# Kernel optimization log

Measured on AMD Instinct MI355X. Metric: run time of the kernel, lower is better.

## Reference

```python
import jax, jax.numpy as jnp
import numpy as np

KERNEL_SIZE = 3

def setup_inputs() -> dict:
    key = jax.random.key(0)
    x = jax.random.normal(key, (16, 64, 128, 128), dtype=jnp.float32)
    return {"x": x}

def reference(x) -> jnp.ndarray:
    # im2col / sliding-window patch extraction with zero padding (SAME).
    # out[b, h, w, c, i, j] = pad(x)[b, c, h + i, w + j]
    k = KERNEL_SIZE
    p = k // 2
    B, C, H, W = x.shape
    xp = jnp.pad(x, ((0, 0), (0, 0), (p, p), (p, p)))  # (B, C, H+2p, W+2p)
    # k*k = 9 static slices (not a data-dim loop), stacked into one tensor.
    patches = jnp.stack(
        [xp[:, :, i:i + H, j:j + W] for i in range(k) for j in range(k)],
        axis=-1,
    )  # (B, C, H, W, k*k)
    patches = patches.reshape(B, C, H, W, k, k)
    return patches.transpose(0, 2, 3, 1, 4, 5)  # (B, H, W, C, k, k)
```

## Files before the change

### kernel.cpp

```cpp
#include <hip/hip_runtime.h>


typedef float f4 __attribute__((ext_vector_type(4), aligned(4)));

__global__ __launch_bounds__(576)
void im2col_kernel(const float* __restrict__ x, float* __restrict__ out) {
    const int el = threadIdx.x;

    const int bid = blockIdx.x;
    const int R   = ((bid & 7) << 8) + (bid >> 3);
    const int h = R & 127;
    const int b = R >> 7;

    const int c  = el / 9;
    const int ij = el - c * 9;
    const int i  = ij / 3;
    const int j  = ij - i * 3;

    const int row = h + i - 1;
    const bool rv = (unsigned)row < 128u;
    const float* rp = x + ((size_t)b * 64 + c) * 16384 + (rv ? row : 0) * 128;
    const int j1 = j - 1;

    float* ob = out + (size_t)R * (128 * 576) + el;

    {
        int col = j1;
        float v = rp[col < 0 ? 0 : col];
        __builtin_nontemporal_store((rv && col >= 0) ? v : 0.0f, ob);
    }

#pragma unroll 4
    for (int it = 0; it < 31; ++it) {
        int w = 1 + (it << 2);
        f4 v = *(const f4*)(rp + w + j1);
        if (!rv) { v.x = 0.0f; v.y = 0.0f; v.z = 0.0f; v.w = 0.0f; }
        float* o = ob + (size_t)w * 576;
        __builtin_nontemporal_store(v.x, o);
        __builtin_nontemporal_store(v.y, o + 576);
        __builtin_nontemporal_store(v.z, o + 2 * 576);
        __builtin_nontemporal_store(v.w, o + 3 * 576);
    }

#pragma unroll
    for (int w = 125; w < 128; ++w) {
        int col = w + j1;
        float v = rp[col > 127 ? 127 : col];
        __builtin_nontemporal_store((rv && col <= 127) ? v : 0.0f,
                                    ob + (size_t)w * 576);
    }
}

extern "C" void kernel_launch(void* const* d_in, const int* in_sizes, int n_in,
                              void* d_out, int out_size, void* d_ws, size_t ws_size,
                              hipStream_t stream) {
    const float* x = (const float*)d_in[0];
    float* out = (float*)d_out;
    im2col_kernel<<<2048, 576, 0, stream>>>(x, out);
}
```

Baseline: 120.2 us.

## Vectorize output stores by assigning four consecutive channel-patch elements per thread

```diff
diff --git a/kernel.cpp b/kernel.cpp
--- a/kernel.cpp
+++ b/kernel.cpp
@@ -5,49 +5,66 @@
 
 __global__ __launch_bounds__(576)
 void im2col_kernel(const float* __restrict__ x, float* __restrict__ out) {
-    const int el = threadIdx.x;
-
+    const int tid = threadIdx.x;
     const int bid = blockIdx.x;
     const int R   = ((bid & 7) << 8) + (bid >> 3);
     const int h = R & 127;
     const int b = R >> 7;
 
-    const int c  = el / 9;
-    const int ij = el - c * 9;
-    const int i  = ij / 3;
-    const int j  = ij - i * 3;
+    const int p0 = tid / 144;
+    const int q  = tid - p0 * 144;
 
-    const int row = h + i - 1;
-    const bool rv = (unsigned)row < 128u;
-    const float* rp = x + ((size_t)b * 64 + c) * 16384 + (rv ? row : 0) * 128;
-    const int j1 = j - 1;
-
-    float* ob = out + (size_t)R * (128 * 576) + el;
-
-    {
-        int col = j1;
-        float v = rp[col < 0 ? 0 : col];
-        __builtin_nontemporal_store((rv && col >= 0) ? v : 0.0f, ob);
+    const float* ptr[4];
+    int jm1[4];
+    bool rv[4];
+#pragma unroll
+    for (int u = 0; u < 4; ++u) {
+        int el = 4 * q + u;
+        int c  = el / 9;
+        int ij = el - 9 * c;
+        int i  = ij / 3;
+        int j  = ij - 3 * i;
+        int row = h + i - 1;
+        rv[u]  = (unsigned)row < 128u;
+        ptr[u] = x + ((size_t)(b * 64 + c) * 128 + (rv[u] ? row : 0)) * 128;
+        jm1[u] = j - 1;
     }
 
-#pragma unroll 4
-    for (int it = 0; it < 31; ++it) {
-        int w = 1 + (it << 2);
-        f4 v = *(const f4*)(rp + w + j1);
-        if (!rv) { v.x = 0.0f; v.y = 0.0f; v.z = 0.0f; v.w = 0.0f; }
-        float* o = ob + (size_t)w * 576;
-        __builtin_nontemporal_store(v.x, o);
-        __builtin_nontemporal_store(v.y, o + 576);
-        __builtin_nontemporal_store(v.z, o + 2 * 576);
-        __builtin_nontemporal_store(v.w, o + 3 * 576);
-    }
+    float* ob = out + (size_t)R * 73728 + 4 * q;
 
 #pragma unroll
-    for (int w = 125; w < 128; ++w) {
-        int col = w + j1;
-        float v = rp[col > 127 ? 127 : col];
-        __builtin_nontemporal_store((rv && col <= 127) ? v : 0.0f,
-                                    ob + (size_t)w * 576);
+    for (int s = 0; s < 8; ++s) {
+        const int w0 = p0 * 32 + s * 4;
+        if (w0 == 0 || w0 == 124) {
+#pragma unroll
+            for (int k = 0; k < 4; ++k) {
+                f4 o;
+#pragma unroll
+                for (int u = 0; u < 4; ++u) {
+                    int col = w0 + k + jm1[u];
+                    bool cv = (unsigned)col < 128u;
+                    float v = ptr[u][cv ? col : 0];
+                    o[u] = (rv[u] && cv) ? v : 0.0f;
+                }
+                __builtin_nontemporal_store(o, (f4*)(ob + (size_t)(w0 + k) * 576));
+            }
+        } else {
+            f4 win[4];
+#pragma unroll
+            for (int u = 0; u < 4; ++u) {
+                win[u] = *(const f4*)(ptr[u] + w0 + jm1[u]);
+                if (!rv[u]) win[u] = (f4){0.0f, 0.0f, 0.0f, 0.0f};
+            }
+#pragma unroll
+            for (int k = 0; k < 4; ++k) {
+                f4 o;
+                o.x = win[0][k];
+                o.y = win[1][k];
+                o.z = win[2][k];
+                o.w = win[3][k];
+                __builtin_nontemporal_store(o, (f4*)(ob + (size_t)(w0 + k) * 576));
+            }
+        }
     }
 }
 
```

Measured after the change: 152.6 us. 26.9% more time.
